# Performance work log

Measured on AMD Instinct MI355X. Metric: run time of the kernel, lower is better.

## Reference

```python
import jax, jax.numpy as jnp
import numpy as np

LOOPS = 2
NUM_GROUPS = 4
EXPERTS_PER_GROUP = 2
NUM_EXPERTS = NUM_GROUPS * EXPERTS_PER_GROUP
GROUPS_TOP_K = 2
TOP_K = 1
RMS_EPS = 1e-6
EPS = 1e-9


def setup_inputs() -> dict:
    key = jax.random.key(0)
    ks = jax.random.split(key, 6)
    B, S, D, F = 2, 1024, 1024, 2048
    return {
        "z": jax.random.normal(ks[0], (B, S, D), jnp.float32),
        "norm_w": jnp.ones((D,), jnp.float32),
        "w_macro": jax.random.normal(ks[1], (NUM_GROUPS, D), jnp.float32) * (D ** -0.5),
        "w_micro": jax.random.normal(ks[2], (NUM_GROUPS, EXPERTS_PER_GROUP, D), jnp.float32) * (D ** -0.5),
        "w1": jax.random.normal(ks[3], (NUM_EXPERTS, F, D), jnp.float32) * (D ** -0.5),
        "w2": jax.random.normal(ks[4], (NUM_EXPERTS, D, F), jnp.float32) * (F ** -0.5),
    }


def _rmsnorm(x, w):
    return x * jax.lax.rsqrt(jnp.mean(x * x, axis=-1, keepdims=True) + RMS_EPS) * w


def _combine_weights(x_flat, w_macro, w_micro):
    """Dense [T, E] combine matrix equivalent to the sort-based dispatch."""
    T = x_flat.shape[0]
    macro = jax.nn.softmax(x_flat @ w_macro.T, axis=-1)                    # [T, G]
    mvals, midx = jax.lax.top_k(macro, GROUPS_TOP_K)                       # [T, Gk]
    mvals = mvals / (jnp.sum(mvals, axis=-1, keepdims=True) + EPS)
    micro = jax.nn.softmax(jnp.einsum('td,ged->tge', x_flat, w_micro), axis=-1)  # [T, G, Eg]
    uvals, uidx = jax.lax.top_k(micro, TOP_K)                              # [T, G, k]
    uvals = uvals / (jnp.sum(uvals, axis=-1, keepdims=True) + EPS)
    tok = jnp.arange(T)
    combine = jnp.zeros((T, NUM_EXPERTS), x_flat.dtype)
    for s in range(GROUPS_TOP_K):
        g = midx[:, s]                                                     # [T]
        wg = mvals[:, s:s + 1]                                             # [T, 1]
        li = uidx[tok, g]                                                  # [T, k] local expert ids in group g
        lv = uvals[tok, g]                                                 # [T, k]
        eidx = g[:, None] * EXPERTS_PER_GROUP + li                         # [T, k] global expert ids
        combine = combine.at[tok[:, None], eidx].add(lv * wg)
    return combine


def reference(z, norm_w, w_macro, w_micro, w1, w2):
    B, S, D = z.shape
    T = B * S
    for _ in range(LOOPS):
        zn = _rmsnorm(z, norm_w)
        x = zn.reshape(T, D)
        combine = _combine_weights(x, w_macro, w_micro)                    # [T, E]
        # Dense equivalent of gather -> per-expert FFN -> weighted index_add
        h = jax.nn.silu(jnp.einsum('td,efd->tef', x, w1))                  # [T, E, F]
        y = jnp.einsum('tef,edf->ted', h, w2)                              # [T, E, D]
        mixed = jnp.einsum('ted,te->td', y, combine)                       # [T, D]
        z = z + mixed.reshape(B, S, D)
    return z
```

## Files before the change

### kernel.cpp

```cpp
#include <hip/hip_runtime.h>
#include <cstdint>
#include <cstddef>

#define T_TOK 2048
#define DDIM  1024
#define FDIM  2048

typedef __attribute__((ext_vector_type(8))) short bf16x8;
typedef __attribute__((ext_vector_type(4))) float f32x4;

static __device__ __forceinline__ float b2f(unsigned short u) {
  union { unsigned int i; float f; } v; v.i = ((unsigned int)u) << 16; return v.f;
}
static __device__ __forceinline__ unsigned short f2b(float f) {
  unsigned int x = __float_as_uint(f);
  return (unsigned short)((x + 0x7fffu + ((x >> 16) & 1u)) >> 16);
}
static __device__ __forceinline__ unsigned int pack2(float a, float b) {
  return (unsigned int)f2b(a) | ((unsigned int)f2b(b) << 16);
}
static __device__ __forceinline__ void gload_lds16(const void* g, void* l) {
  __builtin_amdgcn_global_load_lds(
      (const __attribute__((address_space(1))) void*)g,
      (__attribute__((address_space(3))) void*)l, 16, 0, 0);
}

__global__ void k_probe(const unsigned int* __restrict__ nw, int* __restrict__ flag) {
  if (threadIdx.x == 0) flag[0] = (nw[0] == 0x3F800000u) ? 0 : 1;
}

__global__ void k_init(const void* __restrict__ zin, float* __restrict__ z32,
                       const int* __restrict__ flag) {
  const int i = blockIdx.x * blockDim.x + threadIdx.x;
  float4 f;
  if (flag[0]) {
    ushort4 u = ((const ushort4*)zin)[i];
    f.x = b2f(u.x); f.y = b2f(u.y); f.z = b2f(u.z); f.w = b2f(u.w);
  } else {
    f = ((const float4*)zin)[i];
  }
  ((float4*)z32)[i] = f;
}

__global__ void k_out(const float* __restrict__ z32, void* __restrict__ out,
                      const int* __restrict__ flag) {
  const int i = blockIdx.x * blockDim.x + threadIdx.x;
  const float4 a = ((const float4*)z32)[i];
  if (flag[0]) {
    ushort4 o; o.x = f2b(a.x); o.y = f2b(a.y); o.z = f2b(a.z); o.w = f2b(a.w);
    ((ushort4*)out)[i] = o;
  } else {
    ((float4*)out)[i] = a;
  }
}

__global__ void k_split(const float* __restrict__ w, unsigned short* __restrict__ hi,
                        unsigned short* __restrict__ lo, const int* __restrict__ flag) {
  if (flag[0]) return;
  const size_t i = (size_t)blockIdx.x * blockDim.x + threadIdx.x;
  const float4 v = ((const float4*)w)[i];
  ushort4 h, l;
  h.x = f2b(v.x); l.x = f2b(v.x - b2f(h.x));
  h.y = f2b(v.y); l.y = f2b(v.y - b2f(h.y));
  h.z = f2b(v.z); l.z = f2b(v.z - b2f(h.z));
  h.w = f2b(v.w); l.w = f2b(v.w - b2f(h.w));
  ((ushort4*)hi)[i] = h;
  ((ushort4*)lo)[i] = l;
}

__global__ void k_rms_route(const float* __restrict__ z32,
                            const void* __restrict__ nw,
                            const void* __restrict__ wmac,
                            const void* __restrict__ wmic,
                            const int* __restrict__ flag,
                            unsigned short* __restrict__ xh,
                            unsigned short* __restrict__ xl,
                            float* __restrict__ logits,
                            const int base)
{
  const int tl = blockIdx.x;
  const int t  = base + tl;
  const int tid = threadIdx.x;
  const int lane = tid & 63, wv = tid >> 6;
  const int isbf = flag[0];
  const float4 zv = ((const float4*)(z32 + (size_t)t * DDIM))[tid];
  float ss = zv.x*zv.x + zv.y*zv.y + zv.z*zv.z + zv.w*zv.w;
  #pragma unroll
  for (int o = 32; o > 0; o >>= 1) ss += __shfl_down(ss, o);
  __shared__ float red[4];
  __shared__ float lred[12][4];
  if (lane == 0) red[wv] = ss;
  __syncthreads();
  const float tot = red[0] + red[1] + red[2] + red[3];
  const float scale = 1.f / sqrtf(tot * (1.f / DDIM) + 1e-6f);
  float4 nwv;
  if (isbf) {
    ushort4 u = ((const ushort4*)nw)[tid];
    nwv.x = b2f(u.x); nwv.y = b2f(u.y); nwv.z = b2f(u.z); nwv.w = b2f(u.w);
  } else {
    nwv = ((const float4*)nw)[tid];
  }
  float4 xn;
  xn.x = zv.x * scale * nwv.x;
  xn.y = zv.y * scale * nwv.y;
  xn.z = zv.z * scale * nwv.z;
  xn.w = zv.w * scale * nwv.w;
  ushort4 h4, l4;
  h4.x = f2b(xn.x); l4.x = f2b(xn.x - b2f(h4.x));
  h4.y = f2b(xn.y); l4.y = f2b(xn.y - b2f(h4.y));
  h4.z = f2b(xn.z); l4.z = f2b(xn.z - b2f(h4.z));
  h4.w = f2b(xn.w); l4.w = f2b(xn.w - b2f(h4.w));
  ((ushort4*)(xh + (size_t)tl * DDIM))[tid] = h4;
  ((ushort4*)(xl + (size_t)tl * DDIM))[tid] = l4;

  float part[12];
  #pragma unroll
  for (int r = 0; r < 4; r++) {
    float4 w;
    if (isbf) {
      ushort4 u = ((const ushort4*)wmac)[r * 256 + tid];
      w.x = b2f(u.x); w.y = b2f(u.y); w.z = b2f(u.z); w.w = b2f(u.w);
    } else {
      w = ((const float4*)wmac)[r * 256 + tid];
    }
    part[r] = xn.x*w.x + xn.y*w.y + xn.z*w.z + xn.w*w.w;
  }
  #pragma unroll
  for (int r = 0; r < 8; r++) {
    float4 w;
    if (isbf) {
      ushort4 u = ((const ushort4*)wmic)[r * 256 + tid];
      w.x = b2f(u.x); w.y = b2f(u.y); w.z = b2f(u.z); w.w = b2f(u.w);
    } else {
      w = ((const float4*)wmic)[r * 256 + tid];
    }
    part[4 + r] = xn.x*w.x + xn.y*w.y + xn.z*w.z + xn.w*w.w;
  }
  #pragma unroll
  for (int r = 0; r < 12; r++) {
    float v = part[r];
    #pragma unroll
    for (int o = 32; o > 0; o >>= 1) v += __shfl_down(v, o);
    if (lane == 0) lred[r][wv] = v;
  }
  __syncthreads();
  if (tid < 12)
    logits[tl * 12 + tid] = lred[tid][0] + lred[tid][1] + lred[tid][2] + lred[tid][3];
}

__global__ void k_route_a(const float* __restrict__ logits, int* __restrict__ eidx,
                          float* __restrict__ cw, int* __restrict__ counts, const int Tc)
{
  const int t = blockIdx.x * 256 + threadIdx.x;
  if (t >= Tc) return;
  const float* lg = logits + t * 12;
  float p[4];
  float m = fmaxf(fmaxf(lg[0], lg[1]), fmaxf(lg[2], lg[3]));
  float s = 0.f;
  #pragma unroll
  for (int i = 0; i < 4; i++) { p[i] = expf(lg[i] - m); s += p[i]; }
  #pragma unroll
  for (int i = 0; i < 4; i++) p[i] /= s;
  int i1 = 0;
  #pragma unroll
  for (int i = 1; i < 4; i++) if (p[i] > p[i1]) i1 = i;
  int i2 = (i1 == 0) ? 1 : 0;
  #pragma unroll
  for (int i = 0; i < 4; i++) if (i != i1 && p[i] > p[i2]) i2 = i;
  const float denom = p[i1] + p[i2] + 1e-9f;
  const int gs[2] = { i1, i2 };
  #pragma unroll
  for (int sI = 0; sI < 2; sI++) {
    const int g = gs[sI];
    const float wg = p[g] / denom;
    const float u0 = lg[4 + 2*g], u1 = lg[4 + 2*g + 1];
    const int li = (u1 > u0) ? 1 : 0;
    const float uval = 1.f / (1.f + expf(-fabsf(u0 - u1)));
    const float lv = uval / (uval + 1e-9f);
    const int e = g * 2 + li;
    eidx[t*2 + sI] = e;
    cw[t*2 + sI] = wg * lv;
    atomicAdd(&counts[e], 1);
  }
}

__global__ void k_route_b(const int* __restrict__ counts, int* __restrict__ offsets) {
  if (threadIdx.x == 0) {
    int o = 0;
    for (int e = 0; e < 8; e++) { offsets[e] = o; o += counts[e]; }
    offsets[8] = o;
  }
}

__global__ void k_route_c(const int* __restrict__ eidx, const float* __restrict__ cw,
                          const int* __restrict__ offsets, int* __restrict__ counts2,
                          int* __restrict__ tok, float* __restrict__ wof, const int Tc)
{
  const int t = blockIdx.x * 256 + threadIdx.x;
  if (t >= Tc) return;
  #pragma unroll
  for (int sI = 0; sI < 2; sI++) {
    const int e = eidx[t*2 + sI];
    const int pos = atomicAdd(&counts2[e], 1);
    const int a = offsets[e] + pos;
    tok[a] = t;
    wof[a] = cw[t*2 + sI];
  }
}

template<int KDIM, bool IS_G1, int KSPLIT>
__launch_bounds__(256)
__global__ void k_gemm(const unsigned short* __restrict__ Ah,
                       const unsigned short* __restrict__ Al,
                       const void* __restrict__ Bw,
                       const unsigned short* __restrict__ Bh_pre,
                       const unsigned short* __restrict__ Bl_pre,
                       const int* __restrict__ flag,
                       const int presplit,
                       const int* __restrict__ offsets,
                       const int* __restrict__ tok_of_a,
                       const float* __restrict__ w_of_a,
                       unsigned short* __restrict__ hh_out,
                       unsigned short* __restrict__ hl_out,
                       float* __restrict__ z32,
                       const int Nsize, const int base)
{
  const int gx = gridDim.x, gy = gridDim.y;
  const int nwg = gx * gy * gridDim.z;
  const int bid = blockIdx.x + gx * (blockIdx.y + gy * blockIdx.z);
  const int virt = (bid & 7) * (nwg >> 3) + (bid >> 3);
  const int rblk = virt % gx;
  const int rest = virt / gx;
  const int cblk = rest % gy;
  const int ez   = rest / gy;
  const int e = ez / KSPLIT;
  const int kpart = ez % KSPLIT;

  const int offs = offsets[e];
  const int n_e = offsets[e + 1] - offs;
  const int rbase = rblk * 128;
  if (rbase >= n_e) return;
  const int cbase = cblk * 128;
  const int isbf = flag[0];

  __shared__ __align__(16) unsigned short Ahs[128 * 64];
  __shared__ __align__(16) unsigned short Als[128 * 64];
  __shared__ __align__(16) unsigned short Bhs[128 * 64];
  __shared__ __align__(16) unsigned short Bls[128 * 64];

  const int tid = threadIdx.x;
  const int lane = tid & 63;
  const int wv = tid >> 6;
  const int wr = (wv >> 1) * 64;
  const int wc = (wv & 1) * 64;
  const int lr = lane & 15;
  const int quad = lane >> 4;

  size_t aoff[4], boff[4];
  int gsw[4], loff[4], lbase[4];
  const int ch = tid & 7;
  #pragma unroll
  for (int c = 0; c < 4; c++) {
    const int row = c * 32 + (tid >> 3);
    int rl = rbase + row; if (rl > n_e - 1) rl = n_e - 1;
    if constexpr (IS_G1) aoff[c] = (size_t)tok_of_a[offs + rl] * KDIM;
    else                 aoff[c] = (size_t)(offs + rl) * KDIM;
    boff[c] = ((size_t)e * Nsize + cbase + row) * (size_t)KDIM;
    gsw[c]  = (ch ^ (row & 7)) * 8;
    loff[c] = row * 64 + gsw[c];
    lbase[c] = (c * 32 + wv * 8) * 64;
  }

  f32x4 acc[4][4];
  #pragma unroll
  for (int mt = 0; mt < 4; mt++)
    #pragma unroll
    for (int nt = 0; nt < 4; nt++)
      acc[mt][nt] = (f32x4){0.f, 0.f, 0.f, 0.f};

  const int KCH = KDIM / KSPLIT;
  const int k_lo = kpart * KCH;
  for (int k0 = k_lo; k0 < k_lo + KCH; k0 += 64) {
    __syncthreads();
    #pragma unroll
    for (int c = 0; c < 4; c++) {
      gload_lds16(Ah + aoff[c] + k0 + gsw[c], &Ahs[lbase[c]]);
      gload_lds16(Al + aoff[c] + k0 + gsw[c], &Als[lbase[c]]);
    }
    if (isbf) {
      const unsigned short* B16 = (const unsigned short*)Bw;
      #pragma unroll
      for (int c = 0; c < 4; c++)
        gload_lds16(B16 + boff[c] + k0 + gsw[c], &Bhs[lbase[c]]);
    } else if (presplit) {
      #pragma unroll
      for (int c = 0; c < 4; c++) {
        gload_lds16(Bh_pre + boff[c] + k0 + gsw[c], &Bhs[lbase[c]]);
        gload_lds16(Bl_pre + boff[c] + k0 + gsw[c], &Bls[lbase[c]]);
      }
    } else {
      const float* B32 = (const float*)Bw;
      #pragma unroll
      for (int c = 0; c < 4; c++) {
        const float* bsrc = B32 + boff[c] + k0 + (ch * 8);
        const float4 v0 = *(const float4*)(bsrc);
        const float4 v1 = *(const float4*)(bsrc + 4);
        uint4 bh, bl;
        bh.x = pack2(v0.x, v0.y); bh.y = pack2(v0.z, v0.w);
        bh.z = pack2(v1.x, v1.y); bh.w = pack2(v1.z, v1.w);
        bl.x = pack2(v0.x - b2f((unsigned short)(bh.x & 0xFFFF)), v0.y - b2f((unsigned short)(bh.x >> 16)));
        bl.y = pack2(v0.z - b2f((unsigned short)(bh.y & 0xFFFF)), v0.w - b2f((unsigned short)(bh.y >> 16)));
        bl.z = pack2(v1.x - b2f((unsigned short)(bh.z & 0xFFFF)), v1.y - b2f((unsigned short)(bh.z >> 16)));
        bl.w = pack2(v1.z - b2f((unsigned short)(bh.w & 0xFFFF)), v1.w - b2f((unsigned short)(bh.w >> 16)));
        *(uint4*)(&Bhs[loff[c]]) = bh;
        *(uint4*)(&Bls[loff[c]]) = bl;
      }
    }
    __syncthreads();
    #pragma unroll
    for (int ks = 0; ks < 2; ks++) {
      const int swz = ((ks * 4 + quad) ^ (lr & 7)) * 8;
      bf16x8 af[4], alf[4], bhf[4];
      #pragma unroll
      for (int mt = 0; mt < 4; mt++) {
        const int r = wr + mt * 16 + lr;
        af[mt]  = *(const bf16x8*)(&Ahs[r * 64 + swz]);
        alf[mt] = *(const bf16x8*)(&Als[r * 64 + swz]);
      }
      #pragma unroll
      for (int nt = 0; nt < 4; nt++) {
        const int r = wc + nt * 16 + lr;
        bhf[nt] = *(const bf16x8*)(&Bhs[r * 64 + swz]);
      }
      if (isbf) {
        #pragma unroll
        for (int mt = 0; mt < 4; mt++)
          #pragma unroll
          for (int nt = 0; nt < 4; nt++) {
            acc[mt][nt] = __builtin_amdgcn_mfma_f32_16x16x32_bf16(af[mt],  bhf[nt], acc[mt][nt], 0, 0, 0);
            acc[mt][nt] = __builtin_amdgcn_mfma_f32_16x16x32_bf16(alf[mt], bhf[nt], acc[mt][nt], 0, 0, 0);
          }
      } else {
        bf16x8 blf[4];
        #pragma unroll
        for (int nt = 0; nt < 4; nt++) {
          const int r = wc + nt * 16 + lr;
          blf[nt] = *(const bf16x8*)(&Bls[r * 64 + swz]);
        }
        #pragma unroll
        for (int mt = 0; mt < 4; mt++)
          #pragma unroll
          for (int nt = 0; nt < 4; nt++) {
            acc[mt][nt] = __builtin_amdgcn_mfma_f32_16x16x32_bf16(af[mt],  bhf[nt], acc[mt][nt], 0, 0, 0);
            acc[mt][nt] = __builtin_amdgcn_mfma_f32_16x16x32_bf16(alf[mt], bhf[nt], acc[mt][nt], 0, 0, 0);
            acc[mt][nt] = __builtin_amdgcn_mfma_f32_16x16x32_bf16(af[mt],  blf[nt], acc[mt][nt], 0, 0, 0);
          }
      }
    }
  }

  #pragma unroll
  for (int mt = 0; mt < 4; mt++) {
    #pragma unroll
    for (int reg = 0; reg < 4; reg++) {
      const int rl = rbase + wr + mt * 16 + quad * 4 + reg;
      if (rl < n_e) {
        if constexpr (IS_G1) {
          const size_t ro = (size_t)(offs + rl) * Nsize;
          #pragma unroll
          for (int nt = 0; nt < 4; nt++) {
            const int col = cbase + wc + nt * 16 + lr;
            const float v = acc[mt][nt][reg];
            const float sv = v / (1.f + expf(-v));
            const unsigned short hi = f2b(sv);
            hh_out[ro + col] = hi;
            hl_out[ro + col] = f2b(sv - b2f(hi));
          }
        } else {
          const float w = w_of_a[offs + rl];
          const size_t to = (size_t)(base + tok_of_a[offs + rl]) * Nsize;
          #pragma unroll
          for (int nt = 0; nt < 4; nt++) {
            const int col = cbase + wc + nt * 16 + lr;
            atomicAdd(&z32[to + col], acc[mt][nt][reg] * w);
          }
        }
      }
    }
  }
}

extern "C" void kernel_launch(void* const* d_in, const int* in_sizes, int n_in,
                              void* d_out, int out_size, void* d_ws, size_t ws_size,
                              hipStream_t stream)
{
  (void)in_sizes; (void)n_in; (void)out_size;
  const void* z_in = d_in[0];
  const void* nw   = d_in[1];
  const void* wmac = d_in[2];
  const void* wmic = d_in[3];
  const void* w1   = d_in[4];
  const void* w2   = d_in[5];

  auto rup = [](size_t x) -> size_t { return (x + 255) & ~(size_t)255; };
  auto need = [&](int c) -> size_t {
    size_t Tc = T_TOK / c;
    size_t s = 0;
    s += rup(4);
    s += rup((size_t)T_TOK * DDIM * 4);
    s += rup(Tc * DDIM * 2) * 2;
    s += rup(Tc * 12 * 4);
    s += rup(Tc * 2 * 4) * 2;
    s += 256 + 256;
    s += rup(2 * Tc * 4) * 2;
    s += rup(2 * Tc * (size_t)FDIM * 2) * 2;
    return s;
  };
  const size_t WELEM = (size_t)8 * FDIM * DDIM;
  const size_t wsplit_total = WELEM * 2 * 4;

  int presplit = 0;
  int C;
  if (need(1) + wsplit_total <= ws_size) { C = 1; presplit = 1; }
  else if (need(1) <= ws_size) C = 1;
  else if (need(2) <= ws_size) C = 2;
  else if (need(4) <= ws_size) C = 4;
  else C = 8;
  const int Tc = T_TOK / C;

  char* ws = (char*)d_ws;
  size_t off = 0;
  auto alloc = [&](size_t bytes) -> void* {
    void* p = ws + off;
    off += rup(bytes);
    return p;
  };
  int* flag            = (int*)alloc(4);
  float* z32           = (float*)alloc((size_t)T_TOK * DDIM * 4);
  unsigned short* xh   = (unsigned short*)alloc((size_t)Tc * DDIM * 2);
  unsigned short* xl   = (unsigned short*)alloc((size_t)Tc * DDIM * 2);
  float* logits        = (float*)alloc((size_t)Tc * 12 * 4);
  int* eidx            = (int*)alloc((size_t)Tc * 2 * 4);
  float* cw            = (float*)alloc((size_t)Tc * 2 * 4);
  int* counts          = (int*)alloc(64);
  int* offsets         = (int*)alloc(64);
  int* tok             = (int*)alloc((size_t)2 * Tc * 4);
  float* wof           = (float*)alloc((size_t)2 * Tc * 4);
  unsigned short* hh   = (unsigned short*)alloc((size_t)2 * Tc * FDIM * 2);
  unsigned short* hl   = (unsigned short*)alloc((size_t)2 * Tc * FDIM * 2);
  unsigned short *w1h = nullptr, *w1l = nullptr, *w2h = nullptr, *w2l = nullptr;
  if (presplit) {
    w1h = (unsigned short*)alloc(WELEM * 2);
    w1l = (unsigned short*)alloc(WELEM * 2);
    w2h = (unsigned short*)alloc(WELEM * 2);
    w2l = (unsigned short*)alloc(WELEM * 2);
  }

  k_probe<<<1, 64, 0, stream>>>((const unsigned int*)nw, flag);
  k_init<<<T_TOK * DDIM / 1024, 256, 0, stream>>>(z_in, z32, flag);
  if (presplit) {
    const int sb = (int)(WELEM / 4 / 256);
    k_split<<<sb, 256, 0, stream>>>((const float*)w1, w1h, w1l, flag);
    k_split<<<sb, 256, 0, stream>>>((const float*)w2, w2h, w2l, flag);
  }
  for (int L = 0; L < 2; L++) {
    for (int cb = 0; cb < C; cb++) {
      const int base = cb * Tc;
      hipMemsetAsync(counts, 0, 64, stream);
      k_rms_route<<<Tc, 256, 0, stream>>>(z32, nw, wmac, wmic, flag, xh, xl, logits, base);
      k_route_a<<<Tc / 256, 256, 0, stream>>>(logits, eidx, cw, counts, Tc);
      k_route_b<<<1, 64, 0, stream>>>(counts, offsets);
      k_route_c<<<Tc / 256, 256, 0, stream>>>(eidx, cw, offsets, counts + 8, tok, wof, Tc);
      k_gemm<DDIM, true, 1><<<dim3(Tc / 128, FDIM / 128, 8), 256, 0, stream>>>(
          xh, xl, w1, w1h, w1l, flag, presplit, offsets, tok, nullptr, hh, hl, nullptr, FDIM, base);
      k_gemm<FDIM, false, 2><<<dim3(Tc / 128, DDIM / 128, 16), 256, 0, stream>>>(
          hh, hl, w2, w2h, w2l, flag, presplit, offsets, tok, wof, nullptr, nullptr, z32, DDIM, base);
    }
  }
  k_out<<<T_TOK * DDIM / 1024, 256, 0, stream>>>(z32, d_out, flag);
}
```

Measured before the change: 609.8 us.

## Double-buffer LDS staging with K=32 tiles and split hi/lo waits in presplit GEMM

Replaces the single-buffered K=64 LDS tile with two K=32 buffers so the next tile's global-to-LDS loads are issued while MFMAs run on the current one. Hi parts are loaded first and consumed after a partial vmcnt wait, and lo parts are consumed after a second wait. Wave priority is raised around MFMA blocks and the LDS swizzle changes to match the 32-wide rows. The change aims to hide global load latency behind compute, at the cost of twice as many barriers per K element and hand-tuned waitcnt counts that must match the issue order.

```diff
diff --git a/kernel.cpp b/kernel.cpp
--- a/kernel.cpp
+++ b/kernel.cpp
@@ -243,10 +243,10 @@
   const int cbase = cblk * 128;
   const int isbf = flag[0];
 
-  __shared__ __align__(16) unsigned short Ahs[128 * 64];
-  __shared__ __align__(16) unsigned short Als[128 * 64];
-  __shared__ __align__(16) unsigned short Bhs[128 * 64];
-  __shared__ __align__(16) unsigned short Bls[128 * 64];
+  __shared__ __align__(16) unsigned short Ahs[2][128 * 32];
+  __shared__ __align__(16) unsigned short Als[2][128 * 32];
+  __shared__ __align__(16) unsigned short Bhs[2][128 * 32];
+  __shared__ __align__(16) unsigned short Bls[2][128 * 32];
 
   const int tid = threadIdx.x;
   const int lane = tid & 63;
@@ -256,20 +256,21 @@
   const int lr = lane & 15;
   const int quad = lane >> 4;
 
-  size_t aoff[4], boff[4];
-  int gsw[4], loff[4], lbase[4];
-  const int ch = tid & 7;
-  #pragma unroll
-  for (int c = 0; c < 4; c++) {
-    const int row = c * 32 + (tid >> 3);
+  const int ch2 = tid & 3;
+  const int gsw = ((ch2 ^ ((tid >> 3) & 3)) * 8);
+  size_t aoff2[2], boff2[2];
+  int loff2[2], lbase2[2];
+  #pragma unroll
+  for (int c = 0; c < 2; c++) {
+    const int row = c * 64 + (tid >> 2);
     int rl = rbase + row; if (rl > n_e - 1) rl = n_e - 1;
-    if constexpr (IS_G1) aoff[c] = (size_t)tok_of_a[offs + rl] * KDIM;
-    else                 aoff[c] = (size_t)(offs + rl) * KDIM;
-    boff[c] = ((size_t)e * Nsize + cbase + row) * (size_t)KDIM;
-    gsw[c]  = (ch ^ (row & 7)) * 8;
-    loff[c] = row * 64 + gsw[c];
-    lbase[c] = (c * 32 + wv * 8) * 64;
-  }
+    if constexpr (IS_G1) aoff2[c] = (size_t)tok_of_a[offs + rl] * KDIM;
+    else                 aoff2[c] = (size_t)(offs + rl) * KDIM;
+    boff2[c] = ((size_t)e * Nsize + cbase + row) * (size_t)KDIM;
+    loff2[c] = row * 32 + gsw;
+    lbase2[c] = (c * 64 + wv * 16) * 32;
+  }
+  const int rsl = (quad ^ ((lr >> 1) & 3)) * 8;
 
   f32x4 acc[4][4];
   #pragma unroll
@@ -280,58 +281,111 @@
 
   const int KCH = KDIM / KSPLIT;
   const int k_lo = kpart * KCH;
-  for (int k0 = k_lo; k0 < k_lo + KCH; k0 += 64) {
-    __syncthreads();
-    #pragma unroll
-    for (int c = 0; c < 4; c++) {
-      gload_lds16(Ah + aoff[c] + k0 + gsw[c], &Ahs[lbase[c]]);
-      gload_lds16(Al + aoff[c] + k0 + gsw[c], &Als[lbase[c]]);
+  const int k_hi = k_lo + KCH;
+
+#define STAGE8(B, K0) do {                                                        \
+    _Pragma("unroll")                                                             \
+    for (int c = 0; c < 2; c++)                                                   \
+      gload_lds16(Ah + aoff2[c] + (K0) + gsw, &Ahs[B][lbase2[c]]);                \
+    _Pragma("unroll")                                                             \
+    for (int c = 0; c < 2; c++)                                                   \
+      gload_lds16(Bh_pre + boff2[c] + (K0) + gsw, &Bhs[B][lbase2[c]]);            \
+    _Pragma("unroll")                                                             \
+    for (int c = 0; c < 2; c++)                                                   \
+      gload_lds16(Al + aoff2[c] + (K0) + gsw, &Als[B][lbase2[c]]);                \
+    _Pragma("unroll")                                                             \
+    for (int c = 0; c < 2; c++)                                                   \
+      gload_lds16(Bl_pre + boff2[c] + (K0) + gsw, &Bls[B][lbase2[c]]);            \
+  } while (0)
+
+  if (presplit && !isbf) {
+    bf16x8 af[4], alf[4], bhf[4], blf[4];
+    STAGE8(0, k_lo);
+    int cur = 0;
+    for (int k0 = k_lo; k0 < k_hi; k0 += 32) {
+      const bool notlast = (k0 + 32 < k_hi);
+      asm volatile("s_waitcnt vmcnt(4)" ::: "memory");
+      __builtin_amdgcn_sched_barrier(0);
+      __builtin_amdgcn_s_barrier();
+      __builtin_amdgcn_sched_barrier(0);
+      if (notlast) STAGE8(cur ^ 1, k0 + 32);
+      #pragma unroll
+      for (int mt = 0; mt < 4; mt++)
+        af[mt] = *(const bf16x8*)(&Ahs[cur][(wr + mt * 16 + lr) * 32 + rsl]);
+      #pragma unroll
+      for (int nt = 0; nt < 4; nt++)
+        bhf[nt] = *(const bf16x8*)(&Bhs[cur][(wc + nt * 16 + lr) * 32 + rsl]);
+      __builtin_amdgcn_s_setprio(1);
+      #pragma unroll
+      for (int mt = 0; mt < 4; mt++)
+        #pragma unroll
+        for (int nt = 0; nt < 4; nt++)
+          acc[mt][nt] = __builtin_amdgcn_mfma_f32_16x16x32_bf16(af[mt], bhf[nt], acc[mt][nt], 0, 0, 0);
+      __builtin_amdgcn_s_setprio(0);
+      if (notlast) asm volatile("s_waitcnt vmcnt(8)" ::: "memory");
+      else         asm volatile("s_waitcnt vmcnt(0)" ::: "memory");
+      __builtin_amdgcn_sched_barrier(0);
+      __builtin_amdgcn_s_barrier();
+      __builtin_amdgcn_sched_barrier(0);
+      #pragma unroll
+      for (int mt = 0; mt < 4; mt++)
+        alf[mt] = *(const bf16x8*)(&Als[cur][(wr + mt * 16 + lr) * 32 + rsl]);
+      #pragma unroll
+      for (int nt = 0; nt < 4; nt++)
+        blf[nt] = *(const bf16x8*)(&Bls[cur][(wc + nt * 16 + lr) * 32 + rsl]);
+      __builtin_amdgcn_s_setprio(1);
+      #pragma unroll
+      for (int mt = 0; mt < 4; mt++)
+        #pragma unroll
+        for (int nt = 0; nt < 4; nt++) {
+          acc[mt][nt] = __builtin_amdgcn_mfma_f32_16x16x32_bf16(alf[mt], bhf[nt], acc[mt][nt], 0, 0, 0);
+          acc[mt][nt] = __builtin_amdgcn_mfma_f32_16x16x32_bf16(af[mt],  blf[nt], acc[mt][nt], 0, 0, 0);
+        }
+      __builtin_amdgcn_s_setprio(0);
+      cur ^= 1;
     }
-    if (isbf) {
-      const unsigned short* B16 = (const unsigned short*)Bw;
-      #pragma unroll
-      for (int c = 0; c < 4; c++)
-        gload_lds16(B16 + boff[c] + k0 + gsw[c], &Bhs[lbase[c]]);
-    } else if (presplit) {
-      #pragma unroll
-      for (int c = 0; c < 4; c++) {
-        gload_lds16(Bh_pre + boff[c] + k0 + gsw[c], &Bhs[lbase[c]]);
-        gload_lds16(Bl_pre + boff[c] + k0 + gsw[c], &Bls[lbase[c]]);
+  } else {
+    for (int k0 = k_lo; k0 < k_hi; k0 += 32) {
+      __syncthreads();
+      #pragma unroll
+      for (int c = 0; c < 2; c++) {
+        gload_lds16(Ah + aoff2[c] + k0 + gsw, &Ahs[0][lbase2[c]]);
+        gload_lds16(Al + aoff2[c] + k0 + gsw, &Als[0][lbase2[c]]);
       }
-    } else {
-      const float* B32 = (const float*)Bw;
-      #pragma unroll
-      for (int c = 0; c < 4; c++) {
-        const float* bsrc = B32 + boff[c] + k0 + (ch * 8);
-        const float4 v0 = *(const float4*)(bsrc);
-        const float4 v1 = *(const float4*)(bsrc + 4);
-        uint4 bh, bl;
-        bh.x = pack2(v0.x, v0.y); bh.y = pack2(v0.z, v0.w);
-        bh.z = pack2(v1.x, v1.y); bh.w = pack2(v1.z, v1.w);
-        bl.x = pack2(v0.x - b2f((unsigned short)(bh.x & 0xFFFF)), v0.y - b2f((unsigned short)(bh.x >> 16)));
-        bl.y = pack2(v0.z - b2f((unsigned short)(bh.y & 0xFFFF)), v0.w - b2f((unsigned short)(bh.y >> 16)));
-        bl.z = pack2(v1.x - b2f((unsigned short)(bh.z & 0xFFFF)), v1.y - b2f((unsigned short)(bh.z >> 16)));
-        bl.w = pack2(v1.z - b2f((unsigned short)(bh.w & 0xFFFF)), v1.w - b2f((unsigned short)(bh.w >> 16)));
-        *(uint4*)(&Bhs[loff[c]]) = bh;
-        *(uint4*)(&Bls[loff[c]]) = bl;
+      if (isbf) {
+        const unsigned short* B16 = (const unsigned short*)Bw;
+        #pragma unroll
+        for (int c = 0; c < 2; c++)
+          gload_lds16(B16 + boff2[c] + k0 + gsw, &Bhs[0][lbase2[c]]);
+      } else {
+        const float* B32 = (const float*)Bw;
+        #pragma unroll
+        for (int c = 0; c < 2; c++) {
+          const float* bsrc = B32 + boff2[c] + k0 + ch2 * 8;
+          const float4 v0 = *(const float4*)(bsrc);
+          const float4 v1 = *(const float4*)(bsrc + 4);
+          uint4 bh, bl;
+          bh.x = pack2(v0.x, v0.y); bh.y = pack2(v0.z, v0.w);
+          bh.z = pack2(v1.x, v1.y); bh.w = pack2(v1.z, v1.w);
+          bl.x = pack2(v0.x - b2f((unsigned short)(bh.x & 0xFFFF)), v0.y - b2f((unsigned short)(bh.x >> 16)));
+          bl.y = pack2(v0.z - b2f((unsigned short)(bh.y & 0xFFFF)), v0.w - b2f((unsigned short)(bh.y >> 16)));
+          bl.z = pack2(v1.x - b2f((unsigned short)(bh.z & 0xFFFF)), v1.y - b2f((unsigned short)(bh.z >> 16)));
+          bl.w = pack2(v1.z - b2f((unsigned short)(bh.w & 0xFFFF)), v1.w - b2f((unsigned short)(bh.w >> 16)));
+          *(uint4*)(&Bhs[0][loff2[c]]) = bh;
+          *(uint4*)(&Bls[0][loff2[c]]) = bl;
+        }
       }
-    }
-    __syncthreads();
-    #pragma unroll
-    for (int ks = 0; ks < 2; ks++) {
-      const int swz = ((ks * 4 + quad) ^ (lr & 7)) * 8;
+      __syncthreads();
       bf16x8 af[4], alf[4], bhf[4];
       #pragma unroll
       for (int mt = 0; mt < 4; mt++) {
         const int r = wr + mt * 16 + lr;
-        af[mt]  = *(const bf16x8*)(&Ahs[r * 64 + swz]);
-        alf[mt] = *(const bf16x8*)(&Als[r * 64 + swz]);
+        af[mt]  = *(const bf16x8*)(&Ahs[0][r * 32 + rsl]);
+        alf[mt] = *(const bf16x8*)(&Als[0][r * 32 + rsl]);
       }
       #pragma unroll
-      for (int nt = 0; nt < 4; nt++) {
-        const int r = wc + nt * 16 + lr;
-        bhf[nt] = *(const bf16x8*)(&Bhs[r * 64 + swz]);
-      }
+      for (int nt = 0; nt < 4; nt++)
+        bhf[nt] = *(const bf16x8*)(&Bhs[0][(wc + nt * 16 + lr) * 32 + rsl]);
       if (isbf) {
         #pragma unroll
         for (int mt = 0; mt < 4; mt++)
@@ -343,10 +397,8 @@
       } else {
         bf16x8 blf[4];
         #pragma unroll
-        for (int nt = 0; nt < 4; nt++) {
-          const int r = wc + nt * 16 + lr;
-          blf[nt] = *(const bf16x8*)(&Bls[r * 64 + swz]);
-        }
+        for (int nt = 0; nt < 4; nt++)
+          blf[nt] = *(const bf16x8*)(&Bls[0][(wc + nt * 16 + lr) * 32 + rsl]);
         #pragma unroll
         for (int mt = 0; mt < 4; mt++)
           #pragma unroll
@@ -358,6 +410,7 @@
       }
     }
   }
+#undef STAGE8
 
   #pragma unroll
   for (int mt = 0; mt < 4; mt++) {
```

Result: slower. 684.5 us (+12.2%).
